# Kernel optimization log

Measured on AMD Instinct MI355X. Metric: run time of the kernel, lower is better.

## Reference

```python
import jax, jax.numpy as jnp
import numpy as np
from jax import lax

NUM_CLASSES = 80
CONF = 0.05
IOU_T = 0.5
K_PER_CLASS = 100   # max_detections_per_class
MAX_DET = 100       # max_detections
BOX_VAR = np.array([0.1, 0.1, 0.2, 0.2], dtype=np.float32)


def make_anchors(H, W):
    """AnchorBox.get_anchors: [x, y, w, h] anchors for strides 8..128."""
    ratios = [0.5, 1.0, 2.0]
    scales = [2.0 ** 0, 2.0 ** (1.0 / 3.0), 2.0 ** (2.0 / 3.0)]
    strides = [8, 16, 32, 64, 128]
    areas = [32.0 ** 2, 64.0 ** 2, 128.0 ** 2, 256.0 ** 2, 512.0 ** 2]
    out = []
    for stride, area in zip(strides, areas):
        fh = int(np.ceil(H / stride)); fw = int(np.ceil(W / stride))
        dims = []
        for r in ratios:
            ah = np.sqrt(area / r); aw = area / ah
            for s in scales:
                dims.append([aw * s, ah * s])
        dims = np.array(dims, dtype=np.float32)              # [9,2]
        rx = (np.arange(fw, dtype=np.float32) + 0.5) * stride
        ry = (np.arange(fh, dtype=np.float32) + 0.5) * stride
        cx, cy = np.meshgrid(rx, ry)                         # [fh,fw]
        centers = np.stack([cx, cy], axis=-1)                # [fh,fw,2]
        centers = np.tile(centers[:, :, None, :], (1, 1, 9, 1))
        d = np.tile(dims[None, None, :, :], (fh, fw, 1, 1))
        out.append(np.concatenate([centers, d], axis=-1).reshape(-1, 4))
    return np.concatenate(out, axis=0).astype(np.float32)   # [N,4]


def _iou_matrix(boxes):
    # boxes: [K,4] corner format (x1,y1,x2,y2)
    lt = jnp.maximum(boxes[:, None, :2], boxes[None, :, :2])
    rb = jnp.minimum(boxes[:, None, 2:], boxes[None, :, 2:])
    inter = jnp.prod(jnp.clip(rb - lt, 0.0), axis=-1)
    area = jnp.prod(boxes[:, 2:] - boxes[:, :2], axis=-1)
    union = area[:, None] + area[None, :] - inter
    return inter / jnp.maximum(union, 1e-8)


def _decode(predictions, anchors):
    box_pred = predictions[..., :4] * jnp.asarray(BOX_VAR)
    xy = box_pred[..., :2] * anchors[:, 2:] + anchors[:, :2]
    wh = jnp.exp(box_pred[..., 2:]) * anchors[:, 2:]
    boxes = jnp.concatenate([xy - wh / 2.0, xy + wh / 2.0], axis=-1)  # [B,N,4] corners
    cls = jax.nn.sigmoid(predictions[..., 4:])                        # [B,N,C]
    return boxes, cls


def _nms_image(boxes, cls_scores):
    # boxes [N,4], cls_scores [N,C]
    rng = jnp.arange(K_PER_CLASS)

    def per_class(scores):  # [N]
        top_s, idx = lax.top_k(scores, K_PER_CLASS)
        cb = boxes[idx]                                      # [K,4]
        iou = lax.stop_gradient(_iou_matrix(cb))
        keep0 = top_s > CONF
        def body(i, keep):
            sup = keep[i] & (iou[i] > IOU_T) & (rng > i)
            return keep & (~sup)
        keep = lax.fori_loop(0, K_PER_CLASS, body, keep0)
        return cb, jnp.where(keep, top_s, -1.0)

    cboxes, cscores = jax.vmap(per_class)(cls_scores.T)      # [C,K,4], [C,K]
    cids = jnp.broadcast_to(jnp.arange(NUM_CLASSES, dtype=jnp.float32)[:, None],
                            (NUM_CLASSES, K_PER_CLASS))
    flat_s = cscores.reshape(-1)
    flat_b = cboxes.reshape(-1, 4)
    flat_c = cids.reshape(-1)
    fs, fi = lax.top_k(flat_s, MAX_DET)
    fb = flat_b[fi]
    fc = flat_c[fi]
    mask = fs > 0.0
    valid = jnp.sum(mask).astype(jnp.int32)
    return (jnp.where(mask[:, None], fb, 0.0),
            jnp.where(mask, fs, 0.0),
            jnp.where(mask, fc, 0.0),
            valid)


def setup_inputs() -> dict:
    key = jax.random.key(0)
    k1, k2 = jax.random.split(key)
    images = jax.random.normal(k1, (8, 512, 512, 3), dtype=jnp.float32)
    predictions = jax.random.normal(k2, (8, 49104, 84), dtype=jnp.float32)
    return {"images": images, "predictions": predictions}


def reference(images, predictions):
    H, W = images.shape[1], images.shape[2]
    anchors = jnp.asarray(make_anchors(H, W))                # [49104,4]
    boxes, cls = _decode(predictions, anchors)
    nmsed_boxes, nmsed_scores, nmsed_classes, valid = jax.vmap(_nms_image)(boxes, cls)
    return nmsed_boxes, nmsed_scores, nmsed_classes, valid
```

## Files before the change

kernel.cpp:

```cpp
#include <hip/hip_runtime.h>
#include <math.h>
#include <stdint.h>

#define NANCH 49104
#define NCLS 80
#define KSEL 100
#define NFLAT (NCLS * KSEL)
#define PREDC 84
#define NB 8
#define ECAP 128
#define BATF4 (NANCH * (PREDC / 4))
#define BPB 256
#define PCAP 16
#define LCAP 16
#define OCAP 64
#define FASTN 512
#define RMAX 8
#define THRL 2.5f

struct DimsTable { float d[5][9][2]; };
struct KT { uint32_t key; int tie; };
typedef unsigned long long u64;

__device__ __forceinline__ uint32_t f2key(float f) {
    uint32_t u = __float_as_uint(f);
    return u ^ (uint32_t((int32_t)u >> 31) | 0x80000000u);
}
__device__ __forceinline__ float key2f(uint32_t k) {
    uint32_t u = (k & 0x80000000u) ? (k ^ 0x80000000u) : ~k;
    return __uint_as_float(u);
}
__device__ __forceinline__ float sigm(float x) { return 1.0f / (1.0f + expf(-x)); }

__device__ __forceinline__ void decode_box(const float4 pv, int n,
                                           const DimsTable& dt, float box[4]) {
    int lev, base, fw, stride;
    if (n < 36864)      { lev = 0; base = 0;     fw = 64; stride = 8;   }
    else if (n < 46080) { lev = 1; base = 36864; fw = 32; stride = 16;  }
    else if (n < 48384) { lev = 2; base = 46080; fw = 16; stride = 32;  }
    else if (n < 48960) { lev = 3; base = 48384; fw = 8;  stride = 64;  }
    else                { lev = 4; base = 48960; fw = 4;  stride = 128; }
    int i = n - base;
    int k = i % 9;
    int cell = i / 9;
    int xq = cell % fw, yq = cell / fw;
    float cx = ((float)xq + 0.5f) * (float)stride;
    float cy = ((float)yq + 0.5f) * (float)stride;
    float aw = dt.d[lev][k][0];
    float ah = dt.d[lev][k][1];
    float tx = __fmul_rn(pv.x, 0.1f);
    float ty = __fmul_rn(pv.y, 0.1f);
    float tw = __fmul_rn(pv.z, 0.2f);
    float th = __fmul_rn(pv.w, 0.2f);
    float px = __fadd_rn(__fmul_rn(tx, aw), cx);
    float py = __fadd_rn(__fmul_rn(ty, ah), cy);
    float pw = __fmul_rn(expf(tw), aw);
    float ph = __fmul_rn(expf(th), ah);
    float hw = __fmul_rn(pw, 0.5f);
    float hh = __fmul_rn(ph, 0.5f);
    box[0] = __fsub_rn(px, hw);
    box[1] = __fsub_rn(py, hh);
    box[2] = __fadd_rn(px, hw);
    box[3] = __fadd_rn(py, hh);
}

template <int NC>
struct alignas(16) SelShT {
    int hist[NC][2048];
    int suffix[256];
    uint32_t candKey[KSEL];
    int candIdx[KSEL];
    uint32_t eIdx[ECAP];
    uint32_t sKey[KSEL];
    int sIdx[KSEL];
    int cntG, cntE, krem, newkrem, digit, flast, rmin;
    uint32_t prefix, thrKey;
};

template <int NC, typename G>
__device__ int block_select(G get, int N, int K, SelShT<NC>& sh) {
    const int tid = threadIdx.x;
    const int wid = tid >> 6;
    int Ksel = (N < K) ? N : K;
    if (Ksel <= 0) return 0;

    if (N <= K) {
        if (tid < N) { KT e = get(tid); sh.candKey[tid] = e.key; sh.candIdx[tid] = e.tie; }
        __syncthreads();
        if (tid < N) {
            uint32_t mk = sh.candKey[tid]; int mi = sh.candIdx[tid];
            int rank = 0;
            for (int j = 0; j < N; ++j) {
                uint32_t kj = sh.candKey[j]; int ij = sh.candIdx[j];
                rank += (kj > mk) || (kj == mk && ij < mi);
            }
            sh.sKey[rank] = mk; sh.sIdx[rank] = mi;
        }
        __syncthreads();
        return Ksel;
    }

    if (tid == 0) { sh.krem = K; sh.prefix = 0; }
    for (int pass = 0; pass < 3; ++pass) {
        const int bins   = (pass == 2) ? 1024 : 2048;
        const int dshift = (pass == 0) ? 21 : (pass == 1 ? 10 : 0);
        const int fshift = (pass == 1) ? 21 : 10;
        const int dmask  = bins - 1;
        if (pass == 0) { for (int j = tid; j < NC * 2048; j += 256) ((int*)sh.hist)[j] = 0; }
        else           { for (int j = tid; j < bins; j += 256) sh.hist[0][j] = 0; }
        __syncthreads();
        const uint32_t pref = sh.prefix;
        for (int i = tid; i < N; i += 256) {
            uint32_t key = get(i).key;
            if (pass == 0) {
                atomicAdd(&sh.hist[(NC > 1) ? wid : 0][(key >> dshift) & dmask], 1);
            } else if ((key >> fshift) == pref) {
                atomicAdd(&sh.hist[0][(key >> dshift) & dmask], 1);
            }
        }
        __syncthreads();
        if (NC > 1 && pass == 0) {
            for (int j = tid; j < bins; j += 256) {
                int s = sh.hist[0][j];
                for (int cc = 1; cc < NC; ++cc) s += sh.hist[cc][j];
                sh.hist[0][j] = s;
            }
            __syncthreads();
        }
        const int cpb = bins / 256;
        const int base = tid * cpb;
        int lsum = 0;
        for (int j = 0; j < cpb; ++j) lsum += sh.hist[0][base + j];
        sh.suffix[tid] = lsum;
        __syncthreads();
        for (int off = 1; off < 256; off <<= 1) {
            int v = (tid + off < 256) ? sh.suffix[tid + off] : 0;
            __syncthreads();
            sh.suffix[tid] += v;
            __syncthreads();
        }
        {
            int cum = sh.suffix[tid] - lsum;
            const int krem = sh.krem;
            for (int j = cpb - 1; j >= 0; --j) {
                int cnt = sh.hist[0][base + j];
                if (cnt > 0 && cum < krem && cum + cnt >= krem) {
                    sh.digit = base + j;
                    sh.newkrem = krem - cum;
                }
                cum += cnt;
            }
        }
        __syncthreads();
        if (tid == 0) {
            sh.krem = sh.newkrem;
            if (pass == 0)      sh.prefix = (uint32_t)sh.digit;
            else if (pass == 1) sh.prefix = (sh.prefix << 11) | (uint32_t)sh.digit;
            else                sh.thrKey = (sh.prefix << 10) | (uint32_t)sh.digit;
        }
        __syncthreads();
    }

    if (tid == 0) { sh.cntG = 0; sh.cntE = 0; }
    __syncthreads();
    const uint32_t thr = sh.thrKey;
    for (int i = tid; i < N; i += 256) {
        KT e = get(i);
        if (e.key > thr) {
            int g = atomicAdd(&sh.cntG, 1);
            sh.candKey[g] = e.key; sh.candIdx[g] = e.tie;
        } else if (e.key == thr) {
            int idx = atomicAdd(&sh.cntE, 1);
            if (idx < ECAP) sh.eIdx[idx] = (uint32_t)e.tie;
        }
    }
    __syncthreads();
    const int need = sh.krem;
    const int nG = K - need;
    if (sh.cntE <= ECAP) {
        const int ce = sh.cntE;
        if (tid < ce) {
            uint32_t my = sh.eIdx[tid];
            int rank = 0;
            for (int j = 0; j < ce; ++j) rank += (sh.eIdx[j] < my);
            if (rank < need) { sh.candKey[nG + rank] = thr; sh.candIdx[nG + rank] = (int)my; }
        }
    } else {
        if (tid == 0) sh.flast = -1;
        __syncthreads();
        for (int t = 0; t < need; ++t) {
            if (tid == 0) sh.rmin = 0x7FFFFFFF;
            __syncthreads();
            const int fl = sh.flast;
            int lmin = 0x7FFFFFFF;
            for (int i = tid; i < N; i += 256) {
                KT e = get(i);
                if (e.key == thr && e.tie > fl) lmin = min(lmin, e.tie);
            }
            atomicMin(&sh.rmin, lmin);
            __syncthreads();
            if (tid == 0) { sh.candKey[nG + t] = thr; sh.candIdx[nG + t] = sh.rmin; sh.flast = sh.rmin; }
            __syncthreads();
        }
    }
    __syncthreads();
    if (tid < K) {
        uint32_t mk = sh.candKey[tid]; int mi = sh.candIdx[tid];
        int rank = 0;
        for (int j = 0; j < K; ++j) {
            uint32_t kj = sh.candKey[j]; int ij = sh.candIdx[j];
            rank += (kj > mk) || (kj == mk && ij < mi);
        }
        sh.sKey[rank] = mk; sh.sIdx[rank] = mi;
    }
    __syncthreads();
    return Ksel;
}

__global__ __launch_bounds__(256) void init_k(int* __restrict__ oflowCnt) {
    for (int x = threadIdx.x; x < NB * NCLS; x += 256) oflowCnt[x] = 0;
}

__device__ __forceinline__ void procf4(float4 p, int v, int b,
                                       int* lcnt, uint2 (*buck)[LCAP],
                                       int* oflowCnt, uint2* oflow) {
    uint32_t q = (uint32_t)v / 21u;
    uint32_t j = (uint32_t)v - q * 21u;
    if (j == 0u) return;
    bool c0 = p.x > THRL, c1 = p.y > THRL, c2 = p.z > THRL, c3 = p.w > THRL;
    if (!(c0 | c1 | c2 | c3)) return;
    uint32_t row = q - (uint32_t)b * (uint32_t)NANCH;
    int cbase = ((int)j - 1) * 4;
    float vv[4] = {p.x, p.y, p.z, p.w};
    bool pp[4] = {c0, c1, c2, c3};
#pragma unroll
    for (int k = 0; k < 4; ++k) {
        if (pp[k]) {
            int c = cbase + k;
            uint32_t key = f2key(sigm(vv[k]));
            int slot = atomicAdd(&lcnt[c], 1);
            if (slot < LCAP) {
                buck[c][slot] = make_uint2(key, row);
            } else {
                int bc = b * NCLS + c;
                int gs = atomicAdd(&oflowCnt[bc], 1);
                if (gs < OCAP) oflow[(size_t)bc * OCAP + gs] = make_uint2(key, row);
            }
        }
    }
}

__global__ __launch_bounds__(256) void cand_scan(const float4* __restrict__ predv,
                                                 uint2* __restrict__ cand2,
                                                 int* __restrict__ cnt2,
                                                 int* __restrict__ oflowCnt,
                                                 uint2* __restrict__ oflow) {
    __shared__ uint2 buck[NCLS][LCAP];
    __shared__ int lcnt[NCLS];

    const int tid = threadIdx.x;
    const int b = blockIdx.x / BPB;
    const int part = blockIdx.x - b * BPB;
    const int CH = (BATF4 + BPB - 1) / BPB;

    for (int j = tid; j < NCLS; j += 256) lcnt[j] = 0;
    __syncthreads();

    int s = b * BATF4 + part * CH;
    int e = b * BATF4 + BATF4;
    if (s + CH < e) e = s + CH;

    int v = s + tid;
    for (; v + 7 * 256 < e; v += 8 * 256) {
        float4 a0 = predv[v];
        float4 a1 = predv[v + 1 * 256];
        float4 a2 = predv[v + 2 * 256];
        float4 a3 = predv[v + 3 * 256];
        float4 a4 = predv[v + 4 * 256];
        float4 a5 = predv[v + 5 * 256];
        float4 a6 = predv[v + 6 * 256];
        float4 a7 = predv[v + 7 * 256];
        procf4(a0, v,           b, lcnt, buck, oflowCnt, oflow);
        procf4(a1, v + 1 * 256, b, lcnt, buck, oflowCnt, oflow);
        procf4(a2, v + 2 * 256, b, lcnt, buck, oflowCnt, oflow);
        procf4(a3, v + 3 * 256, b, lcnt, buck, oflowCnt, oflow);
        procf4(a4, v + 4 * 256, b, lcnt, buck, oflowCnt, oflow);
        procf4(a5, v + 5 * 256, b, lcnt, buck, oflowCnt, oflow);
        procf4(a6, v + 6 * 256, b, lcnt, buck, oflowCnt, oflow);
        procf4(a7, v + 7 * 256, b, lcnt, buck, oflowCnt, oflow);
    }
    for (; v < e; v += 256)
        procf4(predv[v], v, b, lcnt, buck, oflowCnt, oflow);
    __syncthreads();

    if (tid < NCLS) {
        int lc = lcnt[tid];
        if (lc > LCAP) lc = LCAP;
        cnt2[((size_t)b * NCLS + tid) * BPB + part] = lc;
    }
    for (int x = tid; x < NCLS * LCAP; x += 256) {
        int c = x >> 4;
        int k = x & (LCAP - 1);
        int lc = lcnt[c];
        if (lc > LCAP) lc = LCAP;
        if (k < lc)
            cand2[(((size_t)b * NCLS + c) * BPB + part) * PCAP + k] = buck[c][k];
    }
}

__global__ __launch_bounds__(256) void nms_sel(const float* __restrict__ pred,
                                               const uint2* __restrict__ cand2,
                                               const int* __restrict__ cnt2,
                                               const int* __restrict__ oflowCnt,
                                               const uint2* __restrict__ oflow,
                                               float* __restrict__ cls_boxes,
                                               uint32_t* __restrict__ posKeyC,
                                               uint32_t* __restrict__ posFlatC,
                                               int* __restrict__ posCntC,
                                               DimsTable dt) {
    __shared__ SelShT<1> sh;
    __shared__ uint16_t prank[4][FASTN];
    __shared__ float sbox[KSEL][4];
    __shared__ float sarea[KSEL];
    __shared__ int sconf[KSEL];
    __shared__ alignas(16) uint32_t sup[KSEL][4];
    __shared__ uint32_t keepm[4];
    const int c = blockIdx.x;
    const int b = blockIdx.y;
    const int tid = threadIdx.x;
    const int bc = b * NCLS + c;

    int myc = cnt2[(size_t)bc * BPB + tid];
    sh.suffix[tid] = myc;
    __syncthreads();
    for (int off = 1; off < 256; off <<= 1) {
        int v = (tid >= off) ? sh.suffix[tid - off] : 0;
        __syncthreads();
        sh.suffix[tid] += v;
        __syncthreads();
    }
    const int excl = sh.suffix[tid] - myc;
    const int n0 = sh.suffix[255];
    const int of = oflowCnt[bc];
    const int n = n0 + of;

    if (n >= KSEL && n <= FASTN && of <= OCAP) {
        u64* list64 = (u64*)sh.hist;
        const uint2* sl = cand2 + ((size_t)bc * BPB + tid) * PCAP;
        for (int k = 0; k < myc; ++k) {
            uint2 p = sl[k];
            list64[excl + k] = ((u64)p.x << 32) | (u64)(~p.y);
        }
        for (int x = tid; x < of; x += 256) {
            uint2 p = oflow[(size_t)bc * OCAP + x];
            list64[n0 + x] = ((u64)p.x << 32) | (u64)(~p.y);
        }
        __syncthreads();
        const int wid = tid >> 6;
        const int lane = tid & 63;
        u64 cl[RMAX];
        int pr[RMAX];
#pragma unroll
        for (int r = 0; r < RMAX; ++r) {
            int i = r * 64 + lane;
            cl[r] = (i < n) ? list64[i] : 0xFFFFFFFFFFFFFFFFull;
            pr[r] = 0;
        }
        const int js = (wid * n) >> 2;
        const int je = ((wid + 1) * n) >> 2;
        int j = js;
        for (; j + 3 < je; j += 4) {
            u64 o0 = list64[j];
            u64 o1 = list64[j + 1];
            u64 o2 = list64[j + 2];
            u64 o3 = list64[j + 3];
#pragma unroll
            for (int r = 0; r < RMAX; ++r)
                pr[r] += (o0 > cl[r]) + (o1 > cl[r]) + (o2 > cl[r]) + (o3 > cl[r]);
        }
        for (; j < je; ++j) {
            u64 o = list64[j];
#pragma unroll
            for (int r = 0; r < RMAX; ++r) pr[r] += (o > cl[r]);
        }
#pragma unroll
        for (int r = 0; r < RMAX; ++r) {
            int i = r * 64 + lane;
            if (i < n) prank[wid][i] = (uint16_t)pr[r];
        }
        __syncthreads();
        for (int i = tid; i < n; i += 256) {
            int rank = (int)prank[0][i] + (int)prank[1][i]
                     + (int)prank[2][i] + (int)prank[3][i];
            if (rank < KSEL) {
                u64 e = list64[i];
                sh.sKey[rank] = (uint32_t)(e >> 32);
                sh.sIdx[rank] = (int)(~(uint32_t)e);
            }
        }
        __syncthreads();
    } else {
        const float* src = pred + (size_t)b * NANCH * PREDC + 4 + c;
        auto g = [src](int i) { KT e; e.key = f2key(sigm(src[(size_t)i * PREDC])); e.tie = i; return e; };
        block_select<1>(g, NANCH, KSEL, sh);
    }

    for (int x = tid; x < KSEL * 4; x += 256) ((uint32_t*)sup)[x] = 0;
    if (tid < KSEL) {
        int ni = sh.sIdx[tid];
        float4 pv = reinterpret_cast<const float4*>(pred)[((size_t)b * NANCH + ni) * (PREDC / 4)];
        float bx[4]; decode_box(pv, ni, dt, bx);
        sbox[tid][0] = bx[0]; sbox[tid][1] = bx[1];
        sbox[tid][2] = bx[2]; sbox[tid][3] = bx[3];
        sarea[tid] = __fmul_rn(__fsub_rn(bx[2], bx[0]), __fsub_rn(bx[3], bx[1]));
        sconf[tid] = (key2f(sh.sKey[tid]) > 0.05f) ? 1 : 0;
    }
    __syncthreads();

    for (int pidx = tid; pidx < KSEL * KSEL; pidx += 256) {
        int i = pidx / KSEL;
        int jj = pidx - i * KSEL;
        if (jj > i && sconf[i] && sconf[jj]) {
            float x1 = fmaxf(sbox[i][0], sbox[jj][0]);
            float y1 = fmaxf(sbox[i][1], sbox[jj][1]);
            float x2 = fminf(sbox[i][2], sbox[jj][2]);
            float y2 = fminf(sbox[i][3], sbox[jj][3]);
            float iw = fmaxf(__fsub_rn(x2, x1), 0.0f);
            float ih = fmaxf(__fsub_rn(y2, y1), 0.0f);
            float inter = __fmul_rn(iw, ih);
            float uni = __fsub_rn(__fadd_rn(sarea[i], sarea[jj]), inter);
            if (__fdiv_rn(inter, fmaxf(uni, 1e-8f)) > 0.5f)
                atomicOr(&sup[i][jj >> 5], 1u << (jj & 31));
        }
    }
    __syncthreads();

    if (tid < 64) {
        const int l = tid;
        uint4 rowA = *reinterpret_cast<const uint4*>(sup[l]);
        int confA = sconf[l];
        uint4 rowB = make_uint4(0u, 0u, 0u, 0u);
        int confB = 0;
        if (l + 64 < KSEL) {
            rowB = *reinterpret_cast<const uint4*>(sup[l + 64]);
            confB = sconf[l + 64];
        }
        u64 mA = __ballot(confA != 0);
        u64 mB = __ballot(confB != 0);
        uint32_t k0 = (uint32_t)mA, k1 = (uint32_t)(mA >> 32);
        uint32_t k2 = (uint32_t)mB, k3 = (uint32_t)(mB >> 32);
        for (int i = 0; i < KSEL; ++i) {
            uint32_t w = (i < 32) ? k0 : (i < 64) ? k1 : (i < 96) ? k2 : k3;
            if ((w >> (i & 31)) & 1u) {
                uint32_t s0, s1, s2, s3;
                if (i < 64) {
                    s0 = __shfl(rowA.x, i); s1 = __shfl(rowA.y, i);
                    s2 = __shfl(rowA.z, i); s3 = __shfl(rowA.w, i);
                } else {
                    s0 = __shfl(rowB.x, i - 64); s1 = __shfl(rowB.y, i - 64);
                    s2 = __shfl(rowB.z, i - 64); s3 = __shfl(rowB.w, i - 64);
                }
                k0 &= ~s0; k1 &= ~s1; k2 &= ~s2; k3 &= ~s3;
            }
        }
        if (l == 0) {
            keepm[0] = k0; keepm[1] = k1; keepm[2] = k2; keepm[3] = k3;
            posCntC[bc] = __popc(k0) + __popc(k1) + __popc(k2) + __popc(k3);
        }
    }
    __syncthreads();

    if (tid < KSEL) {
        reinterpret_cast<float4*>(cls_boxes)[(size_t)b * NFLAT + c * KSEL + tid] =
            make_float4(sbox[tid][0], sbox[tid][1], sbox[tid][2], sbox[tid][3]);
        int w = tid >> 5, bit = tid & 31;
        if ((keepm[w] >> bit) & 1u) {
            int off = __popc(keepm[w] & ((bit == 0) ? 0u : ((1u << bit) - 1u)));
            for (int ww = 0; ww < w; ++ww) off += __popc(keepm[ww]);
            posKeyC[(size_t)bc * KSEL + off] = sh.sKey[tid];
            posFlatC[(size_t)bc * KSEL + off] = (uint32_t)(c * KSEL + tid);
        }
    }
}

__global__ __launch_bounds__(256) void final_sel(const float* __restrict__ cls_boxes,
                                                 const uint32_t* __restrict__ posKeyC,
                                                 const uint32_t* __restrict__ posFlatC,
                                                 const int* __restrict__ posCntC,
                                                 uint32_t* __restrict__ compKey,
                                                 uint32_t* __restrict__ compFlat,
                                                 float* __restrict__ out) {
    __shared__ SelShT<4> sh;
    const int b = blockIdx.x;
    const int tid = threadIdx.x;

    int myc = (tid < NCLS) ? posCntC[b * NCLS + tid] : 0;
    sh.suffix[tid] = myc;
    __syncthreads();
    for (int off = 1; off < 256; off <<= 1) {
        int v = (tid >= off) ? sh.suffix[tid - off] : 0;
        __syncthreads();
        sh.suffix[tid] += v;
        __syncthreads();
    }
    const int excl = sh.suffix[tid] - myc;
    const int m = sh.suffix[255];
    if (tid < NCLS) {
        const size_t sbase = (size_t)(b * NCLS + tid) * KSEL;
        for (int k = 0; k < myc; ++k) {
            compKey[(size_t)b * NFLAT + excl + k] = posKeyC[sbase + k];
            compFlat[(size_t)b * NFLAT + excl + k] = posFlatC[sbase + k];
        }
    }
    __syncthreads();

    const uint32_t* pk = compKey + (size_t)b * NFLAT;
    const uint32_t* pf = compFlat + (size_t)b * NFLAT;
    auto g = [pk, pf](int i) { KT e; e.key = pk[i]; e.tie = (int)pf[i]; return e; };
    int K = block_select<4>(g, m, KSEL, sh);
    if (tid < KSEL) {
        float4 ob = make_float4(0.f, 0.f, 0.f, 0.f);
        float sv = 0.f, cv = 0.f;
        if (tid < K) {
            sv = key2f(sh.sKey[tid]);
            int flat = sh.sIdx[tid];
            ob = reinterpret_cast<const float4*>(cls_boxes)[(size_t)b * NFLAT + flat];
            cv = (float)(flat / KSEL);
        }
        reinterpret_cast<float4*>(out)[(size_t)b * KSEL + tid] = ob;
        out[NB * KSEL * 4 + b * KSEL + tid] = sv;
        out[NB * KSEL * 5 + b * KSEL + tid] = cv;
    }
    if (tid == 0) out[NB * KSEL * 6 + b] = (float)K;
}

extern "C" void kernel_launch(void* const* d_in, const int* in_sizes, int n_in,
                              void* d_out, int out_size, void* d_ws, size_t ws_size,
                              hipStream_t stream) {
    const float* pred = (const float*)d_in[1];
    float* out = (float*)d_out;

    DimsTable dt;
    const double areasd[5] = {1024.0, 4096.0, 16384.0, 65536.0, 262144.0};
    const double ratios[3] = {0.5, 1.0, 2.0};
    const double scales[3] = {1.0, pow(2.0, 1.0 / 3.0), pow(2.0, 2.0 / 3.0)};
    for (int l = 0; l < 5; ++l)
        for (int ri = 0; ri < 3; ++ri) {
            double ah = sqrt(areasd[l] / ratios[ri]);
            double aw = areasd[l] / ah;
            for (int si = 0; si < 3; ++si) {
                dt.d[l][ri * 3 + si][0] = (float)(aw * scales[si]);
                dt.d[l][ri * 3 + si][1] = (float)(ah * scales[si]);
            }
        }

    char* wsb = (char*)d_ws;
    int* oflowCnt = (int*)wsb;
    int* posCntC  = oflowCnt + NB * NCLS;
    uint2* oflow  = (uint2*)(wsb + 8192);
    uint2* cand2  = oflow + (size_t)NB * NCLS * OCAP;
    int* cnt2     = (int*)(cand2 + (size_t)NB * NCLS * BPB * PCAP);
    float* cls_boxes = (float*)(cnt2 + (size_t)NB * NCLS * BPB);
    uint32_t* posKeyC  = (uint32_t*)(cls_boxes + (size_t)NB * NFLAT * 4);
    uint32_t* posFlatC = posKeyC + (size_t)NB * NFLAT;
    uint32_t* compKey  = posFlatC + (size_t)NB * NFLAT;
    uint32_t* compFlat = compKey + (size_t)NB * NFLAT;

    init_k<<<1, 256, 0, stream>>>(oflowCnt);

    cand_scan<<<NB * BPB, 256, 0, stream>>>(reinterpret_cast<const float4*>(pred),
                                            cand2, cnt2, oflowCnt, oflow);

    dim3 gb(NCLS, NB);
    nms_sel<<<gb, 256, 0, stream>>>(pred, cand2, cnt2, oflowCnt, oflow,
                                    cls_boxes, posKeyC, posFlatC, posCntC, dt);

    final_sel<<<NB, 256, 0, stream>>>(cls_boxes, posKeyC, posFlatC, posCntC,
                                      compKey, compFlat, out);
}
```

Measured before the change: 136.1 us.

## Split final top-k into per-class-group rank sort plus wavefront k-way merge

The final per-image selection, formerly a single block per image doing a three-pass radix select over up to 8000 candidates, is replaced by two kernels. The first ranks and selects top-100 within groups of 5 classes across many blocks. The second merges the 16 sorted lists with a wavefront shuffle-max k-way merge. The nms_sel prefix scan also switches to wave shuffles, and the cand2 layout is transposed so per-thread candidate reads coalesce. This adds a kernel launch and assumes each class group holds at most 512 candidates, which holds since each class contributes at most 100.

```diff
diff --git a/kernel.cpp b/kernel.cpp
--- a/kernel.cpp
+++ b/kernel.cpp
@@ -16,6 +16,8 @@
 #define OCAP 64
 #define FASTN 512
 #define RMAX 8
+#define CGRP 5
+#define NCHUNK (NCLS / CGRP)
 #define THRL 2.5f
 
 struct DimsTable { float d[5][9][2]; };
@@ -64,9 +66,8 @@
     box[3] = __fadd_rn(py, hh);
 }
 
-template <int NC>
-struct alignas(16) SelShT {
-    int hist[NC][2048];
+struct alignas(16) SelSh {
+    int hist[2048];
     int suffix[256];
     uint32_t candKey[KSEL];
     int candIdx[KSEL];
@@ -77,10 +78,9 @@
     uint32_t prefix, thrKey;
 };
 
-template <int NC, typename G>
-__device__ int block_select(G get, int N, int K, SelShT<NC>& sh) {
+template <typename G>
+__device__ int block_select(G get, int N, int K, SelSh& sh) {
     const int tid = threadIdx.x;
-    const int wid = tid >> 6;
     int Ksel = (N < K) ? N : K;
     if (Ksel <= 0) return 0;
 
@@ -106,31 +106,22 @@
         const int dshift = (pass == 0) ? 21 : (pass == 1 ? 10 : 0);
         const int fshift = (pass == 1) ? 21 : 10;
         const int dmask  = bins - 1;
-        if (pass == 0) { for (int j = tid; j < NC * 2048; j += 256) ((int*)sh.hist)[j] = 0; }
-        else           { for (int j = tid; j < bins; j += 256) sh.hist[0][j] = 0; }
+        for (int j = tid; j < bins; j += 256) sh.hist[j] = 0;
         __syncthreads();
         const uint32_t pref = sh.prefix;
         for (int i = tid; i < N; i += 256) {
             uint32_t key = get(i).key;
             if (pass == 0) {
-                atomicAdd(&sh.hist[(NC > 1) ? wid : 0][(key >> dshift) & dmask], 1);
+                atomicAdd(&sh.hist[(key >> dshift) & dmask], 1);
             } else if ((key >> fshift) == pref) {
-                atomicAdd(&sh.hist[0][(key >> dshift) & dmask], 1);
-            }
-        }
-        __syncthreads();
-        if (NC > 1 && pass == 0) {
-            for (int j = tid; j < bins; j += 256) {
-                int s = sh.hist[0][j];
-                for (int cc = 1; cc < NC; ++cc) s += sh.hist[cc][j];
-                sh.hist[0][j] = s;
-            }
-            __syncthreads();
-        }
+                atomicAdd(&sh.hist[(key >> dshift) & dmask], 1);
+            }
+        }
+        __syncthreads();
         const int cpb = bins / 256;
         const int base = tid * cpb;
         int lsum = 0;
-        for (int j = 0; j < cpb; ++j) lsum += sh.hist[0][base + j];
+        for (int j = 0; j < cpb; ++j) lsum += sh.hist[base + j];
         sh.suffix[tid] = lsum;
         __syncthreads();
         for (int off = 1; off < 256; off <<= 1) {
@@ -143,7 +134,7 @@
             int cum = sh.suffix[tid] - lsum;
             const int krem = sh.krem;
             for (int j = cpb - 1; j >= 0; --j) {
-                int cnt = sh.hist[0][base + j];
+                int cnt = sh.hist[base + j];
                 if (cnt > 0 && cum < krem && cum + cnt >= krem) {
                     sh.digit = base + j;
                     sh.newkrem = krem - cum;
@@ -304,7 +295,7 @@
         int lc = lcnt[c];
         if (lc > LCAP) lc = LCAP;
         if (k < lc)
-            cand2[(((size_t)b * NCLS + c) * BPB + part) * PCAP + k] = buck[c][k];
+            cand2[((size_t)(b * NCLS + c) * PCAP + k) * BPB + part] = buck[c][k];
     }
 }
 
@@ -318,8 +309,9 @@
                                                uint32_t* __restrict__ posFlatC,
                                                int* __restrict__ posCntC,
                                                DimsTable dt) {
-    __shared__ SelShT<1> sh;
+    __shared__ SelSh sh;
     __shared__ uint16_t prank[4][FASTN];
+    __shared__ int wtot[4];
     __shared__ float sbox[KSEL][4];
     __shared__ float sarea[KSEL];
     __shared__ int sconf[KSEL];
@@ -329,26 +321,32 @@
     const int b = blockIdx.y;
     const int tid = threadIdx.x;
     const int bc = b * NCLS + c;
+    const int lane = tid & 63;
+    const int wid = tid >> 6;
 
     int myc = cnt2[(size_t)bc * BPB + tid];
-    sh.suffix[tid] = myc;
-    __syncthreads();
-    for (int off = 1; off < 256; off <<= 1) {
-        int v = (tid >= off) ? sh.suffix[tid - off] : 0;
-        __syncthreads();
-        sh.suffix[tid] += v;
-        __syncthreads();
-    }
-    const int excl = sh.suffix[tid] - myc;
-    const int n0 = sh.suffix[255];
+    {
+        int x = myc;
+        for (int off = 1; off < 64; off <<= 1) {
+            int y = __shfl_up(x, off);
+            if (lane >= off) x += y;
+        }
+        if (lane == 63) wtot[wid] = x;
+        __syncthreads();
+        int base = 0;
+#pragma unroll
+        for (int w = 0; w < 4; ++w) if (w < wid) base += wtot[w];
+        sh.suffix[tid] = base + x - myc;
+    }
+    const int excl = sh.suffix[tid];
+    const int n0 = wtot[0] + wtot[1] + wtot[2] + wtot[3];
     const int of = oflowCnt[bc];
     const int n = n0 + of;
 
     if (n >= KSEL && n <= FASTN && of <= OCAP) {
         u64* list64 = (u64*)sh.hist;
-        const uint2* sl = cand2 + ((size_t)bc * BPB + tid) * PCAP;
         for (int k = 0; k < myc; ++k) {
-            uint2 p = sl[k];
+            uint2 p = cand2[((size_t)bc * PCAP + k) * BPB + tid];
             list64[excl + k] = ((u64)p.x << 32) | (u64)(~p.y);
         }
         for (int x = tid; x < of; x += 256) {
@@ -356,8 +354,6 @@
             list64[n0 + x] = ((u64)p.x << 32) | (u64)(~p.y);
         }
         __syncthreads();
-        const int wid = tid >> 6;
-        const int lane = tid & 63;
         u64 cl[RMAX];
         int pr[RMAX];
 #pragma unroll
@@ -402,7 +398,7 @@
     } else {
         const float* src = pred + (size_t)b * NANCH * PREDC + 4 + c;
         auto g = [src](int i) { KT e; e.key = f2key(sigm(src[(size_t)i * PREDC])); e.tie = i; return e; };
-        block_select<1>(g, NANCH, KSEL, sh);
+        block_select(g, NANCH, KSEL, sh);
     }
 
     for (int x = tid; x < KSEL * 4; x += 256) ((uint32_t*)sup)[x] = 0;
@@ -483,55 +479,148 @@
     }
 }
 
-__global__ __launch_bounds__(256) void final_sel(const float* __restrict__ cls_boxes,
-                                                 const uint32_t* __restrict__ posKeyC,
+__global__ __launch_bounds__(256) void chunk_sel(const uint32_t* __restrict__ posKeyC,
                                                  const uint32_t* __restrict__ posFlatC,
                                                  const int* __restrict__ posCntC,
-                                                 uint32_t* __restrict__ compKey,
-                                                 uint32_t* __restrict__ compFlat,
+                                                 u64* __restrict__ chunkOut,
+                                                 int* __restrict__ chunkN) {
+    __shared__ u64 list64[FASTN];
+    __shared__ uint16_t prank[4][FASTN];
+    __shared__ int csh[CGRP + 1];
+    __shared__ u64 osel[KSEL];
+    const int g = blockIdx.x;
+    const int b = blockIdx.y;
+    const int tid = threadIdx.x;
+    const int lane = tid & 63;
+    const int wid = tid >> 6;
+    const int c0 = g * CGRP;
+
+    if (tid == 0) {
+        int acc = 0;
+        for (int cc = 0; cc < CGRP; ++cc) {
+            csh[cc] = acc;
+            acc += posCntC[b * NCLS + c0 + cc];
+        }
+        csh[CGRP] = acc;
+    }
+    __syncthreads();
+    const int n = csh[CGRP];
+
+    for (int idx = tid; idx < CGRP * KSEL; idx += 256) {
+        int cc = idx / KSEL;
+        int k = idx - cc * KSEL;
+        int base = csh[cc];
+        if (k < csh[cc + 1] - base) {
+            size_t sp = (size_t)(b * NCLS + c0 + cc) * KSEL + k;
+            list64[base + k] = ((u64)posKeyC[sp] << 32) | (u64)(~posFlatC[sp]);
+        }
+    }
+    __syncthreads();
+
+    if (n > 0) {
+        u64 cl[RMAX];
+        int pr[RMAX];
+#pragma unroll
+        for (int r = 0; r < RMAX; ++r) {
+            int i = r * 64 + lane;
+            cl[r] = (i < n) ? list64[i] : 0xFFFFFFFFFFFFFFFFull;
+            pr[r] = 0;
+        }
+        const int js = (wid * n) >> 2;
+        const int je = ((wid + 1) * n) >> 2;
+        int j = js;
+        for (; j + 3 < je; j += 4) {
+            u64 o0 = list64[j];
+            u64 o1 = list64[j + 1];
+            u64 o2 = list64[j + 2];
+            u64 o3 = list64[j + 3];
+#pragma unroll
+            for (int r = 0; r < RMAX; ++r)
+                pr[r] += (o0 > cl[r]) + (o1 > cl[r]) + (o2 > cl[r]) + (o3 > cl[r]);
+        }
+        for (; j < je; ++j) {
+            u64 o = list64[j];
+#pragma unroll
+            for (int r = 0; r < RMAX; ++r) pr[r] += (o > cl[r]);
+        }
+#pragma unroll
+        for (int r = 0; r < RMAX; ++r) {
+            int i = r * 64 + lane;
+            if (i < n) prank[wid][i] = (uint16_t)pr[r];
+        }
+        __syncthreads();
+        for (int i = tid; i < n; i += 256) {
+            int rank = (int)prank[0][i] + (int)prank[1][i]
+                     + (int)prank[2][i] + (int)prank[3][i];
+            if (rank < KSEL) osel[rank] = list64[i];
+        }
+    }
+    __syncthreads();
+    const int kn = (n < KSEL) ? n : KSEL;
+    if (tid < kn)
+        chunkOut[(size_t)(b * NCHUNK + g) * KSEL + tid] = osel[tid];
+    if (tid == 0) chunkN[b * NCHUNK + g] = kn;
+}
+
+__global__ __launch_bounds__(256) void merge_sel(const u64* __restrict__ chunkOut,
+                                                 const int* __restrict__ chunkN,
+                                                 const float* __restrict__ cls_boxes,
                                                  float* __restrict__ out) {
-    __shared__ SelShT<4> sh;
+    __shared__ u64 lst[NCHUNK][KSEL];
+    __shared__ int ln[NCHUNK];
+    __shared__ u64 osel[KSEL];
+    __shared__ int okcnt;
     const int b = blockIdx.x;
     const int tid = threadIdx.x;
 
-    int myc = (tid < NCLS) ? posCntC[b * NCLS + tid] : 0;
-    sh.suffix[tid] = myc;
-    __syncthreads();
-    for (int off = 1; off < 256; off <<= 1) {
-        int v = (tid >= off) ? sh.suffix[tid - off] : 0;
-        __syncthreads();
-        sh.suffix[tid] += v;
-        __syncthreads();
-    }
-    const int excl = sh.suffix[tid] - myc;
-    const int m = sh.suffix[255];
-    if (tid < NCLS) {
-        const size_t sbase = (size_t)(b * NCLS + tid) * KSEL;
-        for (int k = 0; k < myc; ++k) {
-            compKey[(size_t)b * NFLAT + excl + k] = posKeyC[sbase + k];
-            compFlat[(size_t)b * NFLAT + excl + k] = posFlatC[sbase + k];
-        }
-    }
-    __syncthreads();
-
-    const uint32_t* pk = compKey + (size_t)b * NFLAT;
-    const uint32_t* pf = compFlat + (size_t)b * NFLAT;
-    auto g = [pk, pf](int i) { KT e; e.key = pk[i]; e.tie = (int)pf[i]; return e; };
-    int K = block_select<4>(g, m, KSEL, sh);
+    if (tid < NCHUNK) ln[tid] = chunkN[b * NCHUNK + tid];
+    if (tid == 0) okcnt = 0;
+    __syncthreads();
+    for (int x = tid; x < NCHUNK * KSEL; x += 256) {
+        int g = x / KSEL;
+        int k = x - g * KSEL;
+        lst[g][k] = (k < ln[g]) ? chunkOut[(size_t)(b * NCHUNK + g) * KSEL + k] : 0ull;
+    }
+    __syncthreads();
+
+    if (tid < 64) {
+        const int l = tid;
+        u64 h = (l < NCHUNK) ? lst[l][0] : 0ull;
+        int p = 0;
+        for (int r = 0; r < KSEL; ++r) {
+            u64 m = h;
+#pragma unroll
+            for (int off = 8; off >= 1; off >>= 1) {
+                u64 o = __shfl_xor(m, off);
+                if (o > m) m = o;
+            }
+            if (l < NCHUNK && h == m && m != 0ull) {
+                ++p;
+                h = (p < ln[l]) ? lst[l][p] : 0ull;
+            }
+            if (l == 0) osel[r] = m;
+        }
+    }
+    __syncthreads();
+
     if (tid < KSEL) {
+        u64 e = osel[tid];
         float4 ob = make_float4(0.f, 0.f, 0.f, 0.f);
         float sv = 0.f, cv = 0.f;
-        if (tid < K) {
-            sv = key2f(sh.sKey[tid]);
-            int flat = sh.sIdx[tid];
+        if (e != 0ull) {
+            uint32_t key = (uint32_t)(e >> 32);
+            int flat = (int)(~(uint32_t)e);
+            sv = key2f(key);
             ob = reinterpret_cast<const float4*>(cls_boxes)[(size_t)b * NFLAT + flat];
             cv = (float)(flat / KSEL);
+            atomicAdd(&okcnt, 1);
         }
         reinterpret_cast<float4*>(out)[(size_t)b * KSEL + tid] = ob;
         out[NB * KSEL * 4 + b * KSEL + tid] = sv;
         out[NB * KSEL * 5 + b * KSEL + tid] = cv;
     }
-    if (tid == 0) out[NB * KSEL * 6 + b] = (float)K;
+    __syncthreads();
+    if (tid == 0) out[NB * KSEL * 6 + b] = (float)okcnt;
 }
 
 extern "C" void kernel_launch(void* const* d_in, const int* in_sizes, int n_in,
@@ -557,14 +646,14 @@
     char* wsb = (char*)d_ws;
     int* oflowCnt = (int*)wsb;
     int* posCntC  = oflowCnt + NB * NCLS;
-    uint2* oflow  = (uint2*)(wsb + 8192);
+    int* chunkNb  = posCntC + NB * NCLS;
+    uint2* oflow  = (uint2*)(wsb + 16384);
     uint2* cand2  = oflow + (size_t)NB * NCLS * OCAP;
-    int* cnt2     = (int*)(cand2 + (size_t)NB * NCLS * BPB * PCAP);
+    int* cnt2     = (int*)(cand2 + (size_t)NB * NCLS * PCAP * BPB);
     float* cls_boxes = (float*)(cnt2 + (size_t)NB * NCLS * BPB);
     uint32_t* posKeyC  = (uint32_t*)(cls_boxes + (size_t)NB * NFLAT * 4);
     uint32_t* posFlatC = posKeyC + (size_t)NB * NFLAT;
-    uint32_t* compKey  = posFlatC + (size_t)NB * NFLAT;
-    uint32_t* compFlat = compKey + (size_t)NB * NFLAT;
+    u64* chunkOut = (u64*)(posFlatC + (size_t)NB * NFLAT);
 
     init_k<<<1, 256, 0, stream>>>(oflowCnt);
 
@@ -575,6 +664,8 @@
     nms_sel<<<gb, 256, 0, stream>>>(pred, cand2, cnt2, oflowCnt, oflow,
                                     cls_boxes, posKeyC, posFlatC, posCntC, dt);
 
-    final_sel<<<NB, 256, 0, stream>>>(cls_boxes, posKeyC, posFlatC, posCntC,
-                                      compKey, compFlat, out);
-}
+    dim3 gc(NCHUNK, NB);
+    chunk_sel<<<gc, 256, 0, stream>>>(posKeyC, posFlatC, posCntC, chunkOut, chunkNb);
+
+    merge_sel<<<NB, 256, 0, stream>>>(chunkOut, chunkNb, cls_boxes, out);
+}
```

Measured after the change: 118.5 us (median of 2 runs). 12.9% less time.
